# Optimization experiments

Measured on AMD Instinct MI355X. Metric: run time of the kernel, lower is better.

The kernel has to match this reference:

```python
import jax, jax.numpy as jnp
import numpy as np

N_NODES = 100000
N_EDGES = 1600000
NFEAT = 256
NHID = 128
NCLASS = 2
NEG_SLOPE = 0.2


def setup_inputs() -> dict:
    key = jax.random.key(0)
    ks = jax.random.split(key, 8)
    x = jax.random.normal(ks[0], (N_NODES, NFEAT), dtype=jnp.float32)
    edge_index = jax.random.randint(ks[1], (2, N_EDGES), 0, N_NODES, dtype=jnp.int64)
    # GATConv params (heads=1): lin weight (no bias), att_src, att_dst, bias
    W = jax.random.normal(ks[2], (NFEAT, NHID), dtype=jnp.float32) * (1.0 / np.sqrt(NFEAT))
    att_src = jax.random.normal(ks[3], (NHID,), dtype=jnp.float32) * (1.0 / np.sqrt(NHID))
    att_dst = jax.random.normal(ks[4], (NHID,), dtype=jnp.float32) * (1.0 / np.sqrt(NHID))
    bias_gat = jnp.zeros((NHID,), dtype=jnp.float32)
    fc_w = jax.random.normal(ks[5], (NCLASS, NHID), dtype=jnp.float32) * (1.0 / np.sqrt(NHID))
    fc_b = jnp.zeros((NCLASS,), dtype=jnp.float32)
    return {"x": x, "edge_index": edge_index, "W": W, "att_src": att_src,
            "att_dst": att_dst, "bias_gat": bias_gat, "fc_w": fc_w, "fc_b": fc_b}


def reference(x, edge_index, W, att_src, att_dst, bias_gat, fc_w, fc_b):
    N = x.shape[0]
    # add self loops (PyG GATConv default)
    loops = jnp.broadcast_to(jnp.arange(N, dtype=edge_index.dtype)[None, :], (2, N))
    ei = jnp.concatenate([edge_index, loops], axis=1)  # [2, E+N]
    src, dst = ei[0], ei[1]

    h = x @ W                                 # [N, NHID]
    a_src = h @ att_src                       # [N]
    a_dst = h @ att_dst                       # [N]

    e = jax.nn.leaky_relu(a_src[src] + a_dst[dst], NEG_SLOPE)  # [E+N]
    # segment softmax over destination nodes (every node has a self loop)
    m = jax.ops.segment_max(e, dst, num_segments=N)
    ex = jnp.exp(e - m[dst])
    s = jax.ops.segment_sum(ex, dst, num_segments=N)
    alpha = ex / (s[dst] + 1e-16)             # [E+N]

    msg = h[src] * alpha[:, None]             # [E+N, NHID]
    out = jax.ops.segment_sum(msg, dst, num_segments=N) + bias_gat  # [N, NHID]

    logits = out @ fc_w.T + fc_b              # [N, NCLASS]
    return jax.nn.log_softmax(logits, axis=1)
```

## Files before the change

### kernel.cpp

```cpp
#include <hip/hip_runtime.h>
#include <hip/hip_bf16.h>
#include <stdint.h>

#define N_NODES 100000
#define N_EDGES 1600000
#define NFEAT   256
#define NHID    128
#define NEG_SLOPE 0.2f

#define NB_B       1563
#define SLAB       2048
#define BIN_BLOCKS 512

typedef __attribute__((ext_vector_type(8))) short short8;
typedef __attribute__((ext_vector_type(4))) float f32x4;

__device__ __forceinline__ int clamp_node(int v) {
    unsigned u = (unsigned)v;
    return (u < (unsigned)N_NODES) ? (int)u : 0;
}

__device__ __forceinline__ unsigned short f2bf(float f) {
    unsigned u = __float_as_uint(f);
    return (unsigned short)((u + 0x7fffu + ((u >> 16) & 1u)) >> 16);
}
__device__ __forceinline__ unsigned pkbf(float a, float b) {
    __hip_bfloat162 t = __float22bfloat162_rn(make_float2(a, b));
    return *reinterpret_cast<unsigned*>(&t);
}
__device__ __forceinline__ float bflo(unsigned p) { return __uint_as_float(p << 16); }
__device__ __forceinline__ float bfhi(unsigned p) { return __uint_as_float(p & 0xffff0000u); }

__global__ __launch_bounds__(256) void k_conv(
    const float* __restrict__ W, unsigned short* __restrict__ Wt)
{
    int id = blockIdx.x * 256 + threadIdx.x;
    int n = id >> 8, k = id & 255;
    Wt[id] = f2bf(W[k * NHID + n]);
}

#define LDS_STRIDE 40
__global__ __launch_bounds__(256) void k_gemm_mfma(
    const float* __restrict__ x,
    const unsigned short* __restrict__ Wt,
    const float* __restrict__ atts,
    const float* __restrict__ attd,
    unsigned short* __restrict__ hb,
    float* __restrict__ asrc,
    float* __restrict__ adst)
{
    __shared__ unsigned short As[128 * LDS_STRIDE];
    __shared__ unsigned short Bs[128 * LDS_STRIDE];
    __shared__ float satt[128][2];

    const int tid  = threadIdx.x;
    const int wave = tid >> 6;
    const int lane = tid & 63;
    const int wm = wave >> 1, wn = wave & 1;
    const int lr = lane & 15, q = lane >> 4;
    const int blockM = blockIdx.x * 128;

    const int sr = tid >> 1;
    const int hh = tid & 1;

    if (tid < 128) { satt[tid][0] = 0.f; satt[tid][1] = 0.f; }

    f32x4 acc[4][4];
#pragma unroll
    for (int a = 0; a < 4; ++a)
#pragma unroll
        for (int b = 0; b < 4; ++b) acc[a][b] = 0.f;

    const int growA = min(blockM + sr, N_NODES - 1);
    const float* xrow = x + (size_t)growA * NFEAT + hh * 16;
    const unsigned short* wrow = Wt + sr * NFEAT + hh * 16;

    float4 va0, va1, va2, va3;
    uint4  vb0, vb1;
    {
        const float4* xp = (const float4*)xrow;
        va0 = xp[0]; va1 = xp[1]; va2 = xp[2]; va3 = xp[3];
        vb0 = *(const uint4*)(wrow);
        vb1 = *(const uint4*)(wrow + 8);
    }

    for (int kt = 0; kt < 8; ++kt) {
        __syncthreads();
        uint4 pa0 = make_uint4(pkbf(va0.x, va0.y), pkbf(va0.z, va0.w),
                               pkbf(va1.x, va1.y), pkbf(va1.z, va1.w));
        uint4 pa1 = make_uint4(pkbf(va2.x, va2.y), pkbf(va2.z, va2.w),
                               pkbf(va3.x, va3.y), pkbf(va3.z, va3.w));
        *(uint4*)&As[sr * LDS_STRIDE + hh * 16 + 0] = pa0;
        *(uint4*)&As[sr * LDS_STRIDE + hh * 16 + 8] = pa1;
        *(uint4*)&Bs[sr * LDS_STRIDE + hh * 16 + 0] = vb0;
        *(uint4*)&Bs[sr * LDS_STRIDE + hh * 16 + 8] = vb1;
        __syncthreads();

        if (kt < 7) {
            const float4* xp = (const float4*)(xrow + (kt + 1) * 32);
            va0 = xp[0]; va1 = xp[1]; va2 = xp[2]; va3 = xp[3];
            vb0 = *(const uint4*)(wrow + (kt + 1) * 32);
            vb1 = *(const uint4*)(wrow + (kt + 1) * 32 + 8);
        }

        short8 af[4], bfr[4];
#pragma unroll
        for (int mt = 0; mt < 4; ++mt)
            af[mt] = *(const short8*)&As[(wm * 64 + mt * 16 + lr) * LDS_STRIDE + q * 8];
#pragma unroll
        for (int nt = 0; nt < 4; ++nt)
            bfr[nt] = *(const short8*)&Bs[(wn * 64 + nt * 16 + lr) * LDS_STRIDE + q * 8];

#pragma unroll
        for (int mt = 0; mt < 4; ++mt)
#pragma unroll
            for (int nt = 0; nt < 4; ++nt)
                acc[mt][nt] = __builtin_amdgcn_mfma_f32_16x16x32_bf16(
                    af[mt], bfr[nt], acc[mt][nt], 0, 0, 0);
    }

    float attsv[4], attdv[4];
#pragma unroll
    for (int nt = 0; nt < 4; ++nt) {
        attsv[nt] = atts[wn * 64 + nt * 16 + lr];
        attdv[nt] = attd[wn * 64 + nt * 16 + lr];
    }
#pragma unroll
    for (int mt = 0; mt < 4; ++mt) {
#pragma unroll
        for (int reg = 0; reg < 4; ++reg) {
            float s = 0.f, d = 0.f;
#pragma unroll
            for (int nt = 0; nt < 4; ++nt) {
                float v = acc[mt][nt][reg];
                s += v * attsv[nt];
                d += v * attdv[nt];
            }
#pragma unroll
            for (int mask = 8; mask > 0; mask >>= 1) {
                s += __shfl_xor(s, mask);
                d += __shfl_xor(d, mask);
            }
            if (lr == 0) {
                int lrow = wm * 64 + mt * 16 + q * 4 + reg;
                atomicAdd(&satt[lrow][0], s);
                atomicAdd(&satt[lrow][1], d);
            }
        }
    }

#pragma unroll
    for (int mt = 0; mt < 4; ++mt) {
#pragma unroll
        for (int reg = 0; reg < 4; ++reg) {
            int grow = blockM + wm * 64 + mt * 16 + q * 4 + reg;
            if (grow < N_NODES) {
                unsigned short* hp = hb + (size_t)grow * NHID + wn * 64 + lr;
#pragma unroll
                for (int nt = 0; nt < 4; ++nt)
                    hp[nt * 16] = f2bf(acc[mt][nt][reg]);
            }
        }
    }

    __syncthreads();
    if (tid < 128) {
        int g = blockM + tid;
        if (g < N_NODES) {
            asrc[g] = satt[tid][0];
            adst[g] = satt[tid][1];
        }
    }
}

__global__ __launch_bounds__(256) void k_bin(
    const int* __restrict__ ei, int* __restrict__ gcur,
    unsigned* __restrict__ staged)
{
    __shared__ int hist[NB_B];
    __shared__ int base[NB_B];
    const int t = threadIdx.x;
    const int per = (N_EDGES + BIN_BLOCKS - 1) / BIN_BLOCKS;
    const int e0 = blockIdx.x * per;
    const int e1 = min(e0 + per, N_EDGES);

    for (int i = t; i < NB_B; i += 256) hist[i] = 0;
    __syncthreads();
    for (int e = e0 + t; e < e1; e += 256)
        atomicAdd(&hist[clamp_node(ei[N_EDGES + e]) >> 6], 1);
    __syncthreads();
    for (int i = t; i < NB_B; i += 256) {
        int c = hist[i];
        base[i] = c ? atomicAdd(&gcur[i], c) : 0;
        hist[i] = 0;
    }
    __syncthreads();
    for (int e = e0 + t; e < e1; e += 256) {
        int d = clamp_node(ei[N_EDGES + e]);
        int s = clamp_node(ei[e]);
        int b = d >> 6;
        int pos = base[b] + atomicAdd(&hist[b], 1);
        if (pos < SLAB)
            staged[(size_t)b * SLAB + pos] = (unsigned)s | ((unsigned)(d & 63) << 17);
    }
}

__global__ __launch_bounds__(256) void k_bsort(
    const unsigned* __restrict__ staged, const int* __restrict__ gcur,
    const float* __restrict__ asrc, const float* __restrict__ adst,
    float2* __restrict__ meta, int* __restrict__ noff, int* __restrict__ ncnt)
{
    __shared__ float2 buf[SLAB];
    __shared__ int hist[64], scanv[64];
    __shared__ float adst_s[64];

    const int b = blockIdx.x;
    const int t = threadIdx.x;
    const int eb = b * SLAB;
    const int n = min(gcur[b], SLAB);
    const int nodeStart = b * 64;

    if (t < 64) {
        hist[t] = 0;
        int gi = nodeStart + t;
        adst_s[t] = (gi < N_NODES) ? adst[gi] : 0.f;
    }
    __syncthreads();

    for (int j = t; j < n; j += 256)
        atomicAdd(&hist[(staged[eb + j] >> 17) & 63], 1);
    __syncthreads();

    if (t < 64) {
        int v = hist[t];
        int sc = v;
#pragma unroll
        for (int off = 1; off < 64; off <<= 1) {
            int u = __shfl_up(sc, off);
            if (t >= off) sc += u;
        }
        scanv[t] = sc - v;
    }
    __syncthreads();

    if (t < 64) {
        int gi = nodeStart + t;
        if (gi < N_NODES) { noff[gi] = eb + scanv[t]; ncnt[gi] = hist[t]; }
        hist[t] = 0;
    }
    __syncthreads();

    for (int j = t; j < n; j += 256) {
        unsigned pk = staged[eb + j];
        int s  = pk & 0x1FFFF;
        int dl = (pk >> 17) & 63;
        float a = asrc[s] + adst_s[dl];
        a = (a > 0.f) ? a : NEG_SLOPE * a;
        float ew = __expf(fminf(a, 60.f));
        int pos = scanv[dl] + atomicAdd(&hist[dl], 1);
        buf[pos] = make_float2(__int_as_float(s), ew);
    }
    __syncthreads();
    for (int j = t; j < n; j += 256) meta[eb + j] = buf[j];
}

__global__ __launch_bounds__(256) void k_agg(
    const unsigned short* __restrict__ hb, const float* __restrict__ asrc,
    const float* __restrict__ adst, const int* __restrict__ noff,
    const int* __restrict__ ncnt, const float2* __restrict__ meta,
    const float* __restrict__ bias, const float* __restrict__ fcw,
    const float* __restrict__ fcb, float* __restrict__ out)
{
    const int wave = threadIdx.x >> 6;
    const int lane = threadIdx.x & 63;
    const int i = blockIdx.x * 4 + wave;
    if (i >= N_NODES) return;

    const unsigned* hrows = (const unsigned*)hb;

    float e0 = asrc[i] + adst[i];
    e0 = (e0 > 0.f) ? e0 : NEG_SLOPE * e0;
    float w = __expf(fminf(e0, 60.f));
    unsigned pself = hrows[(size_t)i * 64 + lane];
    float accx = w * bflo(pself), accy = w * bfhi(pself), ssum = w;

    const int jb = noff[i];
    const int n  = ncnt[i];
    const float2* mp = meta + jb;
    int j = 0;
    for (; j + 8 <= n; j += 8) {
        float2 m[8];
        unsigned p[8];
#pragma unroll
        for (int u = 0; u < 8; ++u) m[u] = mp[j + u];
#pragma unroll
        for (int u = 0; u < 8; ++u)
            p[u] = hrows[(size_t)__float_as_int(m[u].x) * 64 + lane];
#pragma unroll
        for (int u = 0; u < 8; ++u) {
            accx += m[u].y * bflo(p[u]);
            accy += m[u].y * bfhi(p[u]);
            ssum += m[u].y;
        }
    }
    for (; j < n; ++j) {
        float2 m = mp[j];
        unsigned p = hrows[(size_t)__float_as_int(m.x) * 64 + lane];
        accx += m.y * bflo(p);
        accy += m.y * bfhi(p);
        ssum += m.y;
    }

    float inv = 1.0f / (ssum + 1e-16f);
    float ox = accx * inv + bias[2 * lane];
    float oy = accy * inv + bias[2 * lane + 1];

    float l0 = ox * fcw[2 * lane] + oy * fcw[2 * lane + 1];
    float l1 = ox * fcw[NHID + 2 * lane] + oy * fcw[NHID + 2 * lane + 1];
#pragma unroll
    for (int off = 32; off > 0; off >>= 1) {
        l0 += __shfl_down(l0, off);
        l1 += __shfl_down(l1, off);
    }
    if (lane == 0) {
        l0 += fcb[0];
        l1 += fcb[1];
        float m = fmaxf(l0, l1);
        float ls = m + __logf(__expf(l0 - m) + __expf(l1 - m));
        ((float2*)out)[i] = make_float2(l0 - ls, l1 - ls);
    }
}

extern "C" void kernel_launch(void* const* d_in, const int* in_sizes, int n_in,
                              void* d_out, int out_size, void* d_ws, size_t ws_size,
                              hipStream_t stream)
{
    const float* x    = (const float*)d_in[0];
    const int*   ei   = (const int*)d_in[1];
    const float* W    = (const float*)d_in[2];
    const float* atts = (const float*)d_in[3];
    const float* attd = (const float*)d_in[4];
    const float* bias = (const float*)d_in[5];
    const float* fcw  = (const float*)d_in[6];
    const float* fcb  = (const float*)d_in[7];
    float*       out  = (float*)d_out;

    char* base = (char*)d_ws;
    size_t off = 0;
    auto carve = [&](size_t bytes) -> char* {
        char* p = base + off;
        off = (off + bytes + 255) & ~(size_t)255;
        return p;
    };
    unsigned short* hb     = (unsigned short*)carve((size_t)N_NODES * NHID * 2);
    float*          asrc   = (float*)carve(N_NODES * 4);
    float*          adst   = (float*)carve(N_NODES * 4);
    int*            gcur   = (int*)carve(NB_B * 4);
    int*            noff   = (int*)carve(N_NODES * 4);
    int*            ncnt   = (int*)carve(N_NODES * 4);
    unsigned*       staged = (unsigned*)carve((size_t)NB_B * SLAB * 4);
    float2*         meta   = (float2*)carve((size_t)NB_B * SLAB * 8);
    unsigned short* Wt     = (unsigned short*)carve(NHID * NFEAT * 2);
    (void)ws_size; (void)in_sizes; (void)n_in; (void)out_size;

    hipMemsetAsync(gcur, 0, NB_B * 4, stream);

    const int GB = (N_NODES + 127) / 128;

    k_conv<<<(NHID * NFEAT) / 256, 256, 0, stream>>>(W, Wt);
    k_gemm_mfma<<<GB, 256, 0, stream>>>(x, Wt, atts, attd, hb, asrc, adst);
    k_bin<<<BIN_BLOCKS, 256, 0, stream>>>(ei, gcur, staged);
    k_bsort<<<NB_B, 256, 0, stream>>>(staged, gcur, asrc, adst, meta, noff, ncnt);
    k_agg<<<(N_NODES + 3) / 4, 256, 0, stream>>>(hb, asrc, adst, noff, ncnt, meta,
                                                 bias, fcw, fcb, out);
}
```

Measured before the change: 334.5 us.

## Fuse bucket sort and aggregation into one kernel using LDS edge buffer

Result: faster. 311.4 us (-6.9%).

```diff
diff --git a/kernel.cpp b/kernel.cpp
--- a/kernel.cpp
+++ b/kernel.cpp
@@ -205,14 +205,16 @@
     }
 }
 
-__global__ __launch_bounds__(256) void k_bsort(
+__global__ __launch_bounds__(256) void k_sort_agg(
     const unsigned* __restrict__ staged, const int* __restrict__ gcur,
     const float* __restrict__ asrc, const float* __restrict__ adst,
-    float2* __restrict__ meta, int* __restrict__ noff, int* __restrict__ ncnt)
+    const unsigned short* __restrict__ hb,
+    const float* __restrict__ bias, const float* __restrict__ fcw,
+    const float* __restrict__ fcb, float* __restrict__ out)
 {
     __shared__ float2 buf[SLAB];
-    __shared__ int hist[64], scanv[64];
-    __shared__ float adst_s[64];
+    __shared__ int hist[64], scanv[64], cntv[64];
+    __shared__ float asrc_s[64], adst_s[64];
 
     const int b = blockIdx.x;
     const int t = threadIdx.x;
@@ -224,6 +226,7 @@
         hist[t] = 0;
         int gi = nodeStart + t;
         adst_s[t] = (gi < N_NODES) ? adst[gi] : 0.f;
+        asrc_s[t] = (gi < N_NODES) ? asrc[gi] : 0.f;
     }
     __syncthreads();
 
@@ -240,12 +243,7 @@
             if (t >= off) sc += u;
         }
         scanv[t] = sc - v;
-    }
-    __syncthreads();
-
-    if (t < 64) {
-        int gi = nodeStart + t;
-        if (gi < N_NODES) { noff[gi] = eb + scanv[t]; ncnt[gi] = hist[t]; }
+        cntv[t] = v;
         hist[t] = 0;
     }
     __syncthreads();
@@ -261,73 +259,70 @@
         buf[pos] = make_float2(__int_as_float(s), ew);
     }
     __syncthreads();
-    for (int j = t; j < n; j += 256) meta[eb + j] = buf[j];
-}
-
-__global__ __launch_bounds__(256) void k_agg(
-    const unsigned short* __restrict__ hb, const float* __restrict__ asrc,
-    const float* __restrict__ adst, const int* __restrict__ noff,
-    const int* __restrict__ ncnt, const float2* __restrict__ meta,
-    const float* __restrict__ bias, const float* __restrict__ fcw,
-    const float* __restrict__ fcb, float* __restrict__ out)
-{
-    const int wave = threadIdx.x >> 6;
-    const int lane = threadIdx.x & 63;
-    const int i = blockIdx.x * 4 + wave;
-    if (i >= N_NODES) return;
-
+
+    const int wave = t >> 6;
+    const int lane = t & 63;
     const unsigned* hrows = (const unsigned*)hb;
 
-    float e0 = asrc[i] + adst[i];
-    e0 = (e0 > 0.f) ? e0 : NEG_SLOPE * e0;
-    float w = __expf(fminf(e0, 60.f));
-    unsigned pself = hrows[(size_t)i * 64 + lane];
-    float accx = w * bflo(pself), accy = w * bfhi(pself), ssum = w;
-
-    const int jb = noff[i];
-    const int n  = ncnt[i];
-    const float2* mp = meta + jb;
-    int j = 0;
-    for (; j + 8 <= n; j += 8) {
-        float2 m[8];
-        unsigned p[8];
-#pragma unroll
-        for (int u = 0; u < 8; ++u) m[u] = mp[j + u];
-#pragma unroll
-        for (int u = 0; u < 8; ++u)
-            p[u] = hrows[(size_t)__float_as_int(m[u].x) * 64 + lane];
-#pragma unroll
-        for (int u = 0; u < 8; ++u) {
-            accx += m[u].y * bflo(p[u]);
-            accy += m[u].y * bfhi(p[u]);
-            ssum += m[u].y;
-        }
-    }
-    for (; j < n; ++j) {
-        float2 m = mp[j];
-        unsigned p = hrows[(size_t)__float_as_int(m.x) * 64 + lane];
-        accx += m.y * bflo(p);
-        accy += m.y * bfhi(p);
-        ssum += m.y;
-    }
-
-    float inv = 1.0f / (ssum + 1e-16f);
-    float ox = accx * inv + bias[2 * lane];
-    float oy = accy * inv + bias[2 * lane + 1];
-
-    float l0 = ox * fcw[2 * lane] + oy * fcw[2 * lane + 1];
-    float l1 = ox * fcw[NHID + 2 * lane] + oy * fcw[NHID + 2 * lane + 1];
-#pragma unroll
-    for (int off = 32; off > 0; off >>= 1) {
-        l0 += __shfl_down(l0, off);
-        l1 += __shfl_down(l1, off);
-    }
-    if (lane == 0) {
-        l0 += fcb[0];
-        l1 += fcb[1];
-        float m = fmaxf(l0, l1);
-        float ls = m + __logf(__expf(l0 - m) + __expf(l1 - m));
-        ((float2*)out)[i] = make_float2(l0 - ls, l1 - ls);
+    const float b0 = bias[2 * lane], b1 = bias[2 * lane + 1];
+    const float w00 = fcw[2 * lane], w01 = fcw[2 * lane + 1];
+    const float w10 = fcw[NHID + 2 * lane], w11 = fcw[NHID + 2 * lane + 1];
+    const float fb0 = fcb[0], fb1 = fcb[1];
+
+    for (int ln = wave * 16; ln < wave * 16 + 16; ++ln) {
+        int i = nodeStart + ln;
+        if (i >= N_NODES) break;
+
+        float e0 = asrc_s[ln] + adst_s[ln];
+        e0 = (e0 > 0.f) ? e0 : NEG_SLOPE * e0;
+        float w = __expf(fminf(e0, 60.f));
+        unsigned pself = hrows[(unsigned)i * 64u + lane];
+        float accx = w * bflo(pself), accy = w * bfhi(pself), ssum = w;
+
+        const int jb = scanv[ln];
+        const int nn = cntv[ln];
+        int j = 0;
+        for (; j + 8 <= nn; j += 8) {
+            float2 m[8];
+            unsigned p[8];
+#pragma unroll
+            for (int u = 0; u < 8; ++u) m[u] = buf[jb + j + u];
+#pragma unroll
+            for (int u = 0; u < 8; ++u)
+                p[u] = hrows[(unsigned)__float_as_int(m[u].x) * 64u + lane];
+#pragma unroll
+            for (int u = 0; u < 8; ++u) {
+                accx += m[u].y * bflo(p[u]);
+                accy += m[u].y * bfhi(p[u]);
+                ssum += m[u].y;
+            }
+        }
+        for (; j < nn; ++j) {
+            float2 m = buf[jb + j];
+            unsigned p = hrows[(unsigned)__float_as_int(m.x) * 64u + lane];
+            accx += m.y * bflo(p);
+            accy += m.y * bfhi(p);
+            ssum += m.y;
+        }
+
+        float inv = 1.0f / (ssum + 1e-16f);
+        float ox = accx * inv + b0;
+        float oy = accy * inv + b1;
+
+        float l0 = ox * w00 + oy * w01;
+        float l1 = ox * w10 + oy * w11;
+#pragma unroll
+        for (int off = 32; off > 0; off >>= 1) {
+            l0 += __shfl_down(l0, off);
+            l1 += __shfl_down(l1, off);
+        }
+        if (lane == 0) {
+            l0 += fb0;
+            l1 += fb1;
+            float m = fmaxf(l0, l1);
+            float ls = m + __logf(__expf(l0 - m) + __expf(l1 - m));
+            ((float2*)out)[i] = make_float2(l0 - ls, l1 - ls);
+        }
     }
 }
 
@@ -356,10 +351,7 @@
     float*          asrc   = (float*)carve(N_NODES * 4);
     float*          adst   = (float*)carve(N_NODES * 4);
     int*            gcur   = (int*)carve(NB_B * 4);
-    int*            noff   = (int*)carve(N_NODES * 4);
-    int*            ncnt   = (int*)carve(N_NODES * 4);
     unsigned*       staged = (unsigned*)carve((size_t)NB_B * SLAB * 4);
-    float2*         meta   = (float2*)carve((size_t)NB_B * SLAB * 8);
     unsigned short* Wt     = (unsigned short*)carve(NHID * NFEAT * 2);
     (void)ws_size; (void)in_sizes; (void)n_in; (void)out_size;
 
@@ -370,7 +362,6 @@
     k_conv<<<(NHID * NFEAT) / 256, 256, 0, stream>>>(W, Wt);
     k_gemm_mfma<<<GB, 256, 0, stream>>>(x, Wt, atts, attd, hb, asrc, adst);
     k_bin<<<BIN_BLOCKS, 256, 0, stream>>>(ei, gcur, staged);
-    k_bsort<<<NB_B, 256, 0, stream>>>(staged, gcur, asrc, adst, meta, noff, ncnt);
-    k_agg<<<(N_NODES + 3) / 4, 256, 0, stream>>>(hb, asrc, adst, noff, ncnt, meta,
-                                                 bias, fcw, fcb, out);
-}
+    k_sort_agg<<<NB_B, 256, 0, stream>>>(staged, gcur, asrc, adst, hb,
+                                         bias, fcw, fcb, out);
+}
```
